# Optimization experiments

Measured on AMD Instinct MI355X. Metric: run time of the kernel, lower is better.

Reference implementation:

```python
import jax, jax.numpy as jnp
import numpy as np

B, T, D, H = 4, 4096, 4096, 128  # head_size = embedding_size // num_heads = 4096 // 32

def setup_inputs() -> dict:
    key = jax.random.key(0)
    kx, kq, kk, kv = jax.random.split(key, 4)
    x = jax.random.normal(kx, (B, T, D), dtype=jnp.float32)
    # Dense kernels (no bias), init scale 0.01 as in the module
    Wq = jax.random.normal(kq, (D, H), dtype=jnp.float32) * 0.01
    Wk = jax.random.normal(kk, (D, H), dtype=jnp.float32) * 0.01
    Wv = jax.random.normal(kv, (D, H), dtype=jnp.float32) * 0.01
    return {"x": x, "Wq": Wq, "Wk": Wk, "Wv": Wv}

def reference(x, Wq, Wk, Wv):
    # Single-head projections: (B,T,D) @ (D,H) -> (B,T,H)
    Q = jnp.einsum('btd,dh->bth', x, Wq)
    K = jnp.einsum('btd,dh->bth', x, Wk)
    V = jnp.einsum('btd,dh->bth', x, Wv)
    scale = 1.0 / jnp.sqrt(jnp.asarray(H, dtype=Q.dtype))
    scores = jnp.einsum('bth,bsh->bts', Q, K) * scale  # (B,T,S) full score matrix
    weights = jax.nn.softmax(scores, axis=-1)
    # dropout rate = 0.0 (deterministic/eval) -> identity
    out = jnp.einsum('bts,bsh->bth', weights, V)  # (B,T,H)
    return out
```

## Files before the change

kernel.cpp:

```cpp
#include <hip/hip_runtime.h>


typedef __bf16 bf16_t;
typedef bf16_t bf16x8 __attribute__((ext_vector_type(8)));
typedef float f32x4 __attribute__((ext_vector_type(4)));
typedef float f32x8 __attribute__((ext_vector_type(8)));

#define MFMA16(A, B, C) __builtin_amdgcn_mfma_f32_16x16x32_bf16((A), (B), (C), 0, 0, 0)

__device__ __forceinline__ void async_cp16(const bf16_t* g, bf16_t* lds) {
  __builtin_amdgcn_global_load_lds(
      (__attribute__((address_space(1))) unsigned int*)g,
      (__attribute__((address_space(3))) unsigned int*)lds, 16, 0, 0);
}

__global__ void tr_w(const float* __restrict__ w0, const float* __restrict__ w1,
                     const float* __restrict__ w2, bf16_t* __restrict__ wt) {
  __shared__ float tile[32][33];
  const int z = blockIdx.z;
  const float* src = (z == 0) ? w0 : (z == 1) ? w1 : w2;
  bf16_t* dst = wt + (size_t)z * 128 * 4096;
  const int c0 = blockIdx.x * 32;
  const int r0 = blockIdx.y * 32;
  const int tx = threadIdx.x, ty = threadIdx.y;
#pragma unroll
  for (int j = 0; j < 4; ++j)
    tile[ty + 8 * j][tx] = src[(size_t)(r0 + ty + 8 * j) * 128 + c0 + tx];
  __syncthreads();
#pragma unroll
  for (int j = 0; j < 4; ++j)
    dst[(size_t)(c0 + ty + 8 * j) * 4096 + r0 + tx] = (bf16_t)tile[tx][ty + 8 * j];
}

__global__ void tr_v(const bf16_t* __restrict__ v, bf16_t* __restrict__ vt) {
  __shared__ bf16_t tile[32][33];
  const int b = blockIdx.z;
  const bf16_t* src = v + (size_t)b * 4096 * 128;
  bf16_t* dst = vt + (size_t)b * 128 * 4096;
  const int c0 = blockIdx.x * 32;
  const int r0 = blockIdx.y * 32;
  const int tx = threadIdx.x, ty = threadIdx.y;
#pragma unroll
  for (int j = 0; j < 4; ++j)
    tile[ty + 8 * j][tx] = src[(size_t)(r0 + ty + 8 * j) * 128 + c0 + tx];
  __syncthreads();
#pragma unroll
  for (int j = 0; j < 4; ++j)
    dst[(size_t)(c0 + ty + 8 * j) * 4096 + r0 + tx] = tile[tx][ty + 8 * j];
}

__device__ __forceinline__ void stage_b(const bf16_t* __restrict__ wt_k,
                                        bf16_t* sBbuf, int tid) {
#pragma unroll
  for (int r = 0; r < 6; ++r) {
    int cid = r * 512 + tid;
    int n = cid >> 3, pc = cid & 7;
    int lc = pc ^ (n & 7);
    async_cp16(wt_k + (size_t)n * 4096 + lc * 8, sBbuf + (size_t)cid * 8);
  }
}

__launch_bounds__(512, 2)
__global__ void qkv_proj(const float* __restrict__ x, const bf16_t* __restrict__ wt,
                         bf16_t* __restrict__ q, bf16_t* __restrict__ k,
                         bf16_t* __restrict__ v) {
  __shared__ __align__(16) bf16_t sA[2][64 * 64];
  __shared__ __align__(16) bf16_t sB[2][384 * 64];
  const int tid = threadIdx.x;
  const int w = tid >> 6, lane = tid & 63, lq = lane & 15, quad = lane >> 4;
  const int wr = w >> 2, wc = w & 3;
  const int m0 = blockIdx.x * 64;
  const int arow = tid >> 3, apc = tid & 7;
  const int alc = apc ^ (arow & 7);
  const float* xrow = x + (size_t)(m0 + arow) * 4096 + alc * 8;

  f32x4 acc[2][6];
#pragma unroll
  for (int i = 0; i < 2; ++i)
#pragma unroll
    for (int j = 0; j < 6; ++j) acc[i][j] = (f32x4){0.f, 0.f, 0.f, 0.f};

  {
    float4 f0 = ((const float4*)xrow)[0];
    float4 f1 = ((const float4*)xrow)[1];
    stage_b(wt, sB[0], tid);
    f32x8 ff = {f0.x, f0.y, f0.z, f0.w, f1.x, f1.y, f1.z, f1.w};
    *(bf16x8*)(sA[0] + arow * 64 + apc * 8) = __builtin_convertvector(ff, bf16x8);
  }
  __syncthreads();

  for (int kt = 0; kt < 64; ++kt) {
    const int buf = kt & 1;
    float4 f0, f1;
    if (kt < 63) {
      const float* xp = xrow + (kt + 1) * 64;
      f0 = ((const float4*)xp)[0];
      f1 = ((const float4*)xp)[1];
      stage_b(wt + (kt + 1) * 64, sB[buf ^ 1], tid);
    }
#pragma unroll
    for (int ks = 0; ks < 2; ++ks) {
      bf16x8 af[2], bfr[6];
      const int cc = ks * 4 + quad;
#pragma unroll
      for (int mt = 0; mt < 2; ++mt) {
        int row = wr * 32 + mt * 16 + lq;
        af[mt] = *(const bf16x8*)(sA[buf] + row * 64 + ((cc ^ (row & 7)) << 3));
      }
#pragma unroll
      for (int nt = 0; nt < 6; ++nt) {
        int n = wc * 96 + nt * 16 + lq;
        bfr[nt] = *(const bf16x8*)(sB[buf] + n * 64 + ((cc ^ (n & 7)) << 3));
      }
#pragma unroll
      for (int mt = 0; mt < 2; ++mt)
#pragma unroll
        for (int nt = 0; nt < 6; ++nt) acc[mt][nt] = MFMA16(af[mt], bfr[nt], acc[mt][nt]);
    }
    if (kt < 63) {
      f32x8 ff = {f0.x, f0.y, f0.z, f0.w, f1.x, f1.y, f1.z, f1.w};
      *(bf16x8*)(sA[buf ^ 1] + arow * 64 + apc * 8) = __builtin_convertvector(ff, bf16x8);
    }
    __syncthreads();
  }
#pragma unroll
  for (int mt = 0; mt < 2; ++mt) {
#pragma unroll
    for (int nt = 0; nt < 6; ++nt) {
      int n = wc * 96 + nt * 16 + lq;
      bf16_t* dst;
      int nn;
      if (n < 128) { dst = q; nn = n; }
      else if (n < 256) { dst = k; nn = n - 128; }
      else { dst = v; nn = n - 256; }
#pragma unroll
      for (int r = 0; r < 4; ++r) {
        int m = m0 + wr * 32 + mt * 16 + quad * 4 + r;
        dst[(size_t)m * 128 + nn] = (bf16_t)acc[mt][nt][r];
      }
    }
  }
}

__device__ __forceinline__ void stage_kv(const bf16_t* __restrict__ ksrc,
                                         const bf16_t* __restrict__ vsrc,
                                         bf16_t* sKbuf, bf16_t* sVbuf, int tid) {
#pragma unroll
  for (int r = 0; r < 4; ++r) {
    int cid = r * 256 + tid;
    int row = cid >> 4, pc = cid & 15;
    int lc = pc ^ (row & 15);
    async_cp16(ksrc + row * 128 + lc * 8, sKbuf + (size_t)cid * 8);
  }
#pragma unroll
  for (int r = 0; r < 4; ++r) {
    int cid = r * 256 + tid;
    int h = cid >> 3, pc = cid & 7;
    int lc = pc ^ (h & 7);
    async_cp16(vsrc + (size_t)h * 4096 + lc * 8, sVbuf + (size_t)cid * 8);
  }
}

__launch_bounds__(256, 2)
__global__ void flash(const bf16_t* __restrict__ q, const bf16_t* __restrict__ kk,
                      const bf16_t* __restrict__ vt, float* __restrict__ opart,
                      float* __restrict__ mlm, float* __restrict__ mll) {
  __shared__ __align__(16) bf16_t sK[2][64 * 128];
  __shared__ __align__(16) bf16_t sV[2][128 * 64];
  __shared__ __align__(16) bf16_t sP[64 * 72];
  const int tid = threadIdx.x;
  const int w = tid >> 6, lane = tid & 63, lq = lane & 15, quad = lane >> 4;
  const int b = blockIdx.x & 3;
  const int qt = (blockIdx.x >> 2) & 63;
  const int sp = blockIdx.x >> 8;
  const int qrow0 = qt * 64;

  bf16x8 qf[4];
  {
    const bf16_t* qp = q + ((size_t)b * 4096 + qrow0 + w * 16 + lq) * 128 + quad * 8;
#pragma unroll
    for (int ks = 0; ks < 4; ++ks) qf[ks] = *(const bf16x8*)(qp + ks * 32);
  }

  f32x4 accO[8];
#pragma unroll
  for (int i = 0; i < 8; ++i) accO[i] = (f32x4){0.f, 0.f, 0.f, 0.f};
  float mrow[4] = {-1e30f, -1e30f, -1e30f, -1e30f};
  float lrow[4] = {0.f, 0.f, 0.f, 0.f};

  const bf16_t* kbase = kk + (size_t)b * 4096 * 128;
  const bf16_t* vbase = vt + (size_t)b * 128 * 4096;
  const float SCL = 0.08838834764831845f * 1.4426950408889634f;
  const int it0 = sp * 32;

  stage_kv(kbase + (size_t)it0 * 64 * 128, vbase + it0 * 64, sK[0], sV[0], tid);
  __syncthreads();

  for (int i = 0; i < 32; ++i) {
    const int buf = i & 1;
    if (i < 31)
      stage_kv(kbase + (size_t)(it0 + i + 1) * 64 * 128, vbase + (it0 + i + 1) * 64,
               sK[buf ^ 1], sV[buf ^ 1], tid);

    f32x4 accS[4];
#pragma unroll
    for (int nt = 0; nt < 4; ++nt) accS[nt] = (f32x4){0.f, 0.f, 0.f, 0.f};
    __builtin_amdgcn_s_setprio(1);
#pragma unroll
    for (int ks = 0; ks < 4; ++ks) {
      const int cc = ks * 4 + quad;
#pragma unroll
      for (int nt = 0; nt < 4; ++nt) {
        int row = nt * 16 + lq;
        bf16x8 kf = *(const bf16x8*)(sK[buf] + row * 128 + ((cc ^ (row & 15)) << 3));
        accS[nt] = MFMA16(qf[ks], kf, accS[nt]);
      }
    }
    __builtin_amdgcn_s_setprio(0);

    float mxs[4];
#pragma unroll
    for (int r = 0; r < 4; ++r) {
      float t0 = fmaxf(fmaxf(accS[0][r], accS[1][r]), fmaxf(accS[2][r], accS[3][r]));
#pragma unroll
      for (int msk = 1; msk < 16; msk <<= 1) t0 = fmaxf(t0, __shfl_xor(t0, msk));
      mxs[r] = t0 * SCL;
    }
    bool grow = (mxs[0] > mrow[0]) || (mxs[1] > mrow[1]) ||
                (mxs[2] > mrow[2]) || (mxs[3] > mrow[3]);
    if (__any(grow)) {
      float al[4];
#pragma unroll
      for (int r = 0; r < 4; ++r) {
        float mn = fmaxf(mrow[r], mxs[r]);
        al[r] = exp2f(mrow[r] - mn);
        mrow[r] = mn;
        lrow[r] *= al[r];
      }
#pragma unroll
      for (int ot = 0; ot < 8; ++ot) {
        accO[ot][0] *= al[0]; accO[ot][1] *= al[1];
        accO[ot][2] *= al[2]; accO[ot][3] *= al[3];
      }
    }
    float ps[4] = {0.f, 0.f, 0.f, 0.f};
#pragma unroll
    for (int nt = 0; nt < 4; ++nt)
#pragma unroll
      for (int r = 0; r < 4; ++r) {
        float p = exp2f(fmaf(accS[nt][r], SCL, -mrow[r]));
        accS[nt][r] = p;
        ps[r] += p;
      }
#pragma unroll
    for (int r = 0; r < 4; ++r) {
      float s = ps[r];
#pragma unroll
      for (int msk = 1; msk < 16; msk <<= 1) s += __shfl_xor(s, msk);
      lrow[r] += s;
    }

#pragma unroll
    for (int nt = 0; nt < 4; ++nt) {
      int key = nt * 16 + lq;
#pragma unroll
      for (int r = 0; r < 4; ++r) {
        int prow = w * 16 + quad * 4 + r;
        sP[prow * 72 + key] = (bf16_t)accS[nt][r];
      }
    }

    __builtin_amdgcn_s_setprio(1);
#pragma unroll
    for (int ks2 = 0; ks2 < 2; ++ks2) {
      const int cc = ks2 * 4 + quad;
      bf16x8 pf = *(const bf16x8*)(sP + (w * 16 + lq) * 72 + cc * 8);
#pragma unroll
      for (int ot = 0; ot < 8; ++ot) {
        int h = ot * 16 + lq;
        bf16x8 vf = *(const bf16x8*)(sV[buf] + h * 64 + ((cc ^ (h & 7)) << 3));
        accO[ot] = MFMA16(pf, vf, accO[ot]);
      }
    }
    __builtin_amdgcn_s_setprio(0);
    __syncthreads();
  }

  float* op = opart + ((size_t)(sp * 4 + b) * 4096 + qrow0 + w * 16) * 128;
#pragma unroll
  for (int ot = 0; ot < 8; ++ot)
#pragma unroll
    for (int r = 0; r < 4; ++r)
      op[(size_t)(quad * 4 + r) * 128 + ot * 16 + lq] = accO[ot][r];
  if (lq == 0) {
#pragma unroll
    for (int r = 0; r < 4; ++r) {
      size_t idx = (size_t)(sp * 4 + b) * 4096 + qrow0 + w * 16 + quad * 4 + r;
      mlm[idx] = mrow[r];
      mll[idx] = lrow[r];
    }
  }
}

__global__ void merge(const float* __restrict__ opart, const float* __restrict__ mlm,
                      const float* __restrict__ mll, float* __restrict__ out) {
  const int idx = blockIdx.x * 256 + threadIdx.x;
  const int h = idx & 127;
  const int row = idx >> 7;
  float m0 = mlm[row], m1 = mlm[16384 + row];
  float l0 = mll[row], l1 = mll[16384 + row];
  float M = fmaxf(m0, m1);
  float w0 = exp2f(m0 - M), w1 = exp2f(m1 - M);
  float L = w0 * l0 + w1 * l1;
  float acc = w0 * opart[(size_t)row * 128 + h] +
              w1 * opart[((size_t)16384 + row) * 128 + h];
  out[idx] = acc / L;
}

extern "C" void kernel_launch(void* const* d_in, const int* in_sizes, int n_in,
                              void* d_out, int out_size, void* d_ws, size_t ws_size,
                              hipStream_t stream) {
  (void)in_sizes; (void)n_in; (void)out_size; (void)ws_size;
  const float* x  = (const float*)d_in[0];
  const float* wq = (const float*)d_in[1];
  const float* wk = (const float*)d_in[2];
  const float* wv = (const float*)d_in[3];

  char* ws = (char*)d_ws;
  bf16_t* wt  = (bf16_t*)ws;                         ws += (size_t)384 * 4096 * 2;
  bf16_t* qb  = (bf16_t*)ws;                         ws += (size_t)16384 * 128 * 2;
  bf16_t* kb  = (bf16_t*)ws;                         ws += (size_t)16384 * 128 * 2;
  bf16_t* vb  = (bf16_t*)ws;                         ws += (size_t)16384 * 128 * 2;
  bf16_t* vtb = (bf16_t*)ws;                         ws += (size_t)16384 * 128 * 2;
  float*  opart = (float*)ws;                        ws += (size_t)2 * 16384 * 128 * 4;
  float*  mlm = (float*)ws;                          ws += (size_t)2 * 16384 * 4;
  float*  mll = (float*)ws;
  float*  ob  = (float*)d_out;

  dim3 tb(32, 8, 1);
  tr_w<<<dim3(4, 128, 3), tb, 0, stream>>>(wq, wk, wv, wt);
  qkv_proj<<<dim3(256), dim3(512), 0, stream>>>(x, wt, qb, kb, vb);
  tr_v<<<dim3(4, 128, 4), tb, 0, stream>>>(vb, vtb);
  flash<<<dim3(512), dim3(256), 0, stream>>>(qb, kb, vtb, opart, mlm, mll);
  merge<<<dim3(8192), dim3(256), 0, stream>>>(opart, mlm, mll, ob);
}
```

Before: 529.0 us.

## Split QKV projection across N halves and prefetch x two tiles ahead

The QKV projection kernel is relaunched as 512 blocks of 256 threads, with each block computing 192 of the 384 output columns, so twice as many blocks spread over the CUs. The fp32 x tile is now loaded two k-steps ahead in registers and converted into LDS one step ahead. The full __syncthreads is replaced by an explicit partial vmcnt wait plus s_barrier so outstanding x loads can stay in flight. In exchange, each x tile is read twice from global memory (once per N half), and correctness now rests on the hand-written waitcnt counts.

After: 513.8 us. -2.9%, faster.

```diff
diff --git a/kernel.cpp b/kernel.cpp
--- a/kernel.cpp
+++ b/kernel.cpp
@@ -53,26 +53,35 @@
                                         bf16_t* sBbuf, int tid) {
 #pragma unroll
   for (int r = 0; r < 6; ++r) {
-    int cid = r * 512 + tid;
+    int cid = r * 256 + tid;
     int n = cid >> 3, pc = cid & 7;
     int lc = pc ^ (n & 7);
     async_cp16(wt_k + (size_t)n * 4096 + lc * 8, sBbuf + (size_t)cid * 8);
   }
 }
 
-__launch_bounds__(512, 2)
+__launch_bounds__(256, 2)
 __global__ void qkv_proj(const float* __restrict__ x, const bf16_t* __restrict__ wt,
                          bf16_t* __restrict__ q, bf16_t* __restrict__ k,
                          bf16_t* __restrict__ v) {
   __shared__ __align__(16) bf16_t sA[2][64 * 64];
-  __shared__ __align__(16) bf16_t sB[2][384 * 64];
+  __shared__ __align__(16) bf16_t sB[2][192 * 64];
   const int tid = threadIdx.x;
   const int w = tid >> 6, lane = tid & 63, lq = lane & 15, quad = lane >> 4;
-  const int wr = w >> 2, wc = w & 3;
-  const int m0 = blockIdx.x * 64;
-  const int arow = tid >> 3, apc = tid & 7;
-  const int alc = apc ^ (arow & 7);
-  const float* xrow = x + (size_t)(m0 + arow) * 4096 + alc * 8;
+  const int wr = w >> 1, wc = w & 1;
+  const int m0 = (int)(blockIdx.x >> 1) * 64;
+  const int nb = (int)(blockIdx.x & 1) * 192;
+  const bf16_t* wtb = wt + (size_t)nb * 4096;
+
+  int arow[2], apc[2], alc[2];
+#pragma unroll
+  for (int r = 0; r < 2; ++r) {
+    int ca = r * 256 + tid;
+    arow[r] = ca >> 3;
+    apc[r] = ca & 7;
+    alc[r] = apc[r] ^ (arow[r] & 7);
+  }
+  const float* xb = x + (size_t)m0 * 4096;
 
   f32x4 acc[2][6];
 #pragma unroll
@@ -80,23 +89,47 @@
 #pragma unroll
     for (int j = 0; j < 6; ++j) acc[i][j] = (f32x4){0.f, 0.f, 0.f, 0.f};
 
-  {
-    float4 f0 = ((const float4*)xrow)[0];
-    float4 f1 = ((const float4*)xrow)[1];
-    stage_b(wt, sB[0], tid);
-    f32x8 ff = {f0.x, f0.y, f0.z, f0.w, f1.x, f1.y, f1.z, f1.w};
-    *(bf16x8*)(sA[0] + arow * 64 + apc * 8) = __builtin_convertvector(ff, bf16x8);
-  }
-  __syncthreads();
+  float4 fA[4];
+#pragma unroll
+  for (int r = 0; r < 2; ++r) {
+    const float4* p = (const float4*)(xb + (size_t)arow[r] * 4096 + alc[r] * 8);
+    fA[2 * r] = p[0];
+    fA[2 * r + 1] = p[1];
+  }
+  stage_b(wtb, sB[0], tid);
+#pragma unroll
+  for (int r = 0; r < 2; ++r) {
+    f32x8 ff = {fA[2 * r].x, fA[2 * r].y, fA[2 * r].z, fA[2 * r].w,
+                fA[2 * r + 1].x, fA[2 * r + 1].y, fA[2 * r + 1].z, fA[2 * r + 1].w};
+    *(bf16x8*)(sA[0] + arow[r] * 64 + apc[r] * 8) = __builtin_convertvector(ff, bf16x8);
+  }
+#pragma unroll
+  for (int r = 0; r < 2; ++r) {
+    const float4* p = (const float4*)(xb + (size_t)arow[r] * 4096 + 64 + alc[r] * 8);
+    fA[2 * r] = p[0];
+    fA[2 * r + 1] = p[1];
+  }
+  asm volatile("s_waitcnt vmcnt(4) lgkmcnt(0)" ::: "memory");
+  __builtin_amdgcn_s_barrier();
 
   for (int kt = 0; kt < 64; ++kt) {
     const int buf = kt & 1;
-    float4 f0, f1;
-    if (kt < 63) {
-      const float* xp = xrow + (kt + 1) * 64;
-      f0 = ((const float4*)xp)[0];
-      f1 = ((const float4*)xp)[1];
-      stage_b(wt + (kt + 1) * 64, sB[buf ^ 1], tid);
+    const int ktB = (kt < 63) ? kt + 1 : 63;
+    stage_b(wtb + ktB * 64, sB[buf ^ 1], tid);
+#pragma unroll
+    for (int r = 0; r < 2; ++r) {
+      f32x8 ff = {fA[2 * r].x, fA[2 * r].y, fA[2 * r].z, fA[2 * r].w,
+                  fA[2 * r + 1].x, fA[2 * r + 1].y, fA[2 * r + 1].z, fA[2 * r + 1].w};
+      *(bf16x8*)(sA[buf ^ 1] + arow[r] * 64 + apc[r] * 8) =
+          __builtin_convertvector(ff, bf16x8);
+    }
+    const int ktA = (kt < 62) ? kt + 2 : 63;
+#pragma unroll
+    for (int r = 0; r < 2; ++r) {
+      const float4* p =
+          (const float4*)(xb + (size_t)arow[r] * 4096 + ktA * 64 + alc[r] * 8);
+      fA[2 * r] = p[0];
+      fA[2 * r + 1] = p[1];
     }
 #pragma unroll
     for (int ks = 0; ks < 2; ++ks) {
@@ -117,17 +150,14 @@
 #pragma unroll
         for (int nt = 0; nt < 6; ++nt) acc[mt][nt] = MFMA16(af[mt], bfr[nt], acc[mt][nt]);
     }
-    if (kt < 63) {
-      f32x8 ff = {f0.x, f0.y, f0.z, f0.w, f1.x, f1.y, f1.z, f1.w};
-      *(bf16x8*)(sA[buf ^ 1] + arow * 64 + apc * 8) = __builtin_convertvector(ff, bf16x8);
-    }
-    __syncthreads();
+    asm volatile("s_waitcnt vmcnt(4) lgkmcnt(0)" ::: "memory");
+    __builtin_amdgcn_s_barrier();
   }
 #pragma unroll
   for (int mt = 0; mt < 2; ++mt) {
 #pragma unroll
     for (int nt = 0; nt < 6; ++nt) {
-      int n = wc * 96 + nt * 16 + lq;
+      int n = nb + wc * 96 + nt * 16 + lq;
       bf16_t* dst;
       int nn;
       if (n < 128) { dst = q; nn = n; }
@@ -339,7 +369,7 @@
 
   dim3 tb(32, 8, 1);
   tr_w<<<dim3(4, 128, 3), tb, 0, stream>>>(wq, wk, wv, wt);
-  qkv_proj<<<dim3(256), dim3(512), 0, stream>>>(x, wt, qb, kb, vb);
+  qkv_proj<<<dim3(512), dim3(256), 0, stream>>>(x, wt, qb, kb, vb);
   tr_v<<<dim3(4, 128, 4), tb, 0, stream>>>(vb, vtb);
   flash<<<dim3(512), dim3(256), 0, stream>>>(qb, kb, vtb, opart, mlm, mll);
   merge<<<dim3(8192), dim3(256), 0, stream>>>(opart, mlm, mll, ob);
```

## Load A fragments directly to registers and triple-buffer B with explicit waitcnts

Applied to the files above, without the earlier changes.

The QKV projection kernel stops staging x through LDS. Each lane now loads its own MFMA A-fragment fp32 values straight from global memory into registers one k-step ahead and converts them to bf16 there. The weight tiles move to a three-stage LDS ring prefetched two k-steps ahead, synchronised with hand-placed s_waitcnt vmcnt counters and raw s_barrier instead of __syncthreads. This removes the A-tile LDS round trip and is meant to deepen load/compute overlap. The cost is higher LDS use (3x48KB, which may limit occupancy to one block per CU), more registers, and fragile manual vmcnt accounting.

Result: slower. 555.3 us (+5.0%).

```diff
diff --git a/kernel.cpp b/kernel.cpp
--- a/kernel.cpp
+++ b/kernel.cpp
@@ -64,15 +64,16 @@
 __global__ void qkv_proj(const float* __restrict__ x, const bf16_t* __restrict__ wt,
                          bf16_t* __restrict__ q, bf16_t* __restrict__ k,
                          bf16_t* __restrict__ v) {
-  __shared__ __align__(16) bf16_t sA[2][64 * 64];
-  __shared__ __align__(16) bf16_t sB[2][384 * 64];
+  __shared__ __align__(16) bf16_t sB[3][384 * 64];
   const int tid = threadIdx.x;
   const int w = tid >> 6, lane = tid & 63, lq = lane & 15, quad = lane >> 4;
   const int wr = w >> 2, wc = w & 3;
   const int m0 = blockIdx.x * 64;
-  const int arow = tid >> 3, apc = tid & 7;
-  const int alc = apc ^ (arow & 7);
-  const float* xrow = x + (size_t)(m0 + arow) * 4096 + alc * 8;
+
+  const float* abase[2];
+#pragma unroll
+  for (int mt = 0; mt < 2; ++mt)
+    abase[mt] = x + (size_t)(m0 + wr * 32 + mt * 16 + lq) * 4096 + quad * 8;
 
   f32x4 acc[2][6];
 #pragma unroll
@@ -80,49 +81,69 @@
 #pragma unroll
     for (int j = 0; j < 6; ++j) acc[i][j] = (f32x4){0.f, 0.f, 0.f, 0.f};
 
-  {
-    float4 f0 = ((const float4*)xrow)[0];
-    float4 f1 = ((const float4*)xrow)[1];
-    stage_b(wt, sB[0], tid);
-    f32x8 ff = {f0.x, f0.y, f0.z, f0.w, f1.x, f1.y, f1.z, f1.w};
-    *(bf16x8*)(sA[0] + arow * 64 + apc * 8) = __builtin_convertvector(ff, bf16x8);
-  }
-  __syncthreads();
-
+  float4 fAr[8];
+#define LOADA(KT)                                                         \
+  {                                                                       \
+    _Pragma("unroll") for (int mt = 0; mt < 2; ++mt) {                    \
+      _Pragma("unroll") for (int ks = 0; ks < 2; ++ks) {                  \
+        const float4* p = (const float4*)(abase[mt] + (KT)*64 + ks * 32); \
+        fAr[(mt * 2 + ks) * 2 + 0] = p[0];                                \
+        fAr[(mt * 2 + ks) * 2 + 1] = p[1];                                \
+      }                                                                   \
+    }                                                                     \
+  }
+
+  stage_b(wt, sB[0], tid);
+  __builtin_amdgcn_sched_barrier(0);
+  LOADA(0);
+  __builtin_amdgcn_sched_barrier(0);
+  stage_b(wt + 64, sB[1], tid);
+  __builtin_amdgcn_sched_barrier(0);
+  asm volatile("s_waitcnt vmcnt(14)" ::: "memory");
+  __builtin_amdgcn_s_barrier();
+
+  int cur = 0;
   for (int kt = 0; kt < 64; ++kt) {
-    const int buf = kt & 1;
-    float4 f0, f1;
-    if (kt < 63) {
-      const float* xp = xrow + (kt + 1) * 64;
-      f0 = ((const float4*)xp)[0];
-      f1 = ((const float4*)xp)[1];
-      stage_b(wt + (kt + 1) * 64, sB[buf ^ 1], tid);
-    }
+    asm volatile("s_waitcnt vmcnt(6)" ::: "memory");
+    __builtin_amdgcn_sched_barrier(0);
+    bf16x8 af[2][2];
+#pragma unroll
+    for (int mt = 0; mt < 2; ++mt)
+#pragma unroll
+      for (int ks = 0; ks < 2; ++ks) {
+        float4 a = fAr[(mt * 2 + ks) * 2 + 0], b = fAr[(mt * 2 + ks) * 2 + 1];
+        f32x8 ff = {a.x, a.y, a.z, a.w, b.x, b.y, b.z, b.w};
+        af[mt][ks] = __builtin_convertvector(ff, bf16x8);
+      }
+    const int ktA = (kt < 63) ? kt + 1 : 63;
+    LOADA(ktA);
+    __builtin_amdgcn_sched_barrier(0);
+    const int ktB = (kt < 62) ? kt + 2 : 63;
+    const int stg = (cur < 1) ? cur + 2 : cur - 1;
+    stage_b(wt + ktB * 64, sB[stg], tid);
+    __builtin_amdgcn_sched_barrier(0);
+    const bf16_t* sBc = sB[cur];
 #pragma unroll
     for (int ks = 0; ks < 2; ++ks) {
-      bf16x8 af[2], bfr[6];
+      bf16x8 bfr[6];
       const int cc = ks * 4 + quad;
-#pragma unroll
-      for (int mt = 0; mt < 2; ++mt) {
-        int row = wr * 32 + mt * 16 + lq;
-        af[mt] = *(const bf16x8*)(sA[buf] + row * 64 + ((cc ^ (row & 7)) << 3));
-      }
 #pragma unroll
       for (int nt = 0; nt < 6; ++nt) {
         int n = wc * 96 + nt * 16 + lq;
-        bfr[nt] = *(const bf16x8*)(sB[buf] + n * 64 + ((cc ^ (n & 7)) << 3));
+        bfr[nt] = *(const bf16x8*)(sBc + n * 64 + ((cc ^ (n & 7)) << 3));
       }
 #pragma unroll
       for (int mt = 0; mt < 2; ++mt)
 #pragma unroll
-        for (int nt = 0; nt < 6; ++nt) acc[mt][nt] = MFMA16(af[mt], bfr[nt], acc[mt][nt]);
-    }
-    if (kt < 63) {
-      f32x8 ff = {f0.x, f0.y, f0.z, f0.w, f1.x, f1.y, f1.z, f1.w};
-      *(bf16x8*)(sA[buf ^ 1] + arow * 64 + apc * 8) = __builtin_convertvector(ff, bf16x8);
-    }
-    __syncthreads();
-  }
+        for (int nt = 0; nt < 6; ++nt)
+          acc[mt][nt] = MFMA16(af[mt][ks], bfr[nt], acc[mt][nt]);
+    }
+    asm volatile("s_waitcnt vmcnt(14) lgkmcnt(0)" ::: "memory");
+    __builtin_amdgcn_s_barrier();
+    cur = (cur < 2) ? cur + 1 : 0;
+  }
+#undef LOADA
+
 #pragma unroll
   for (int mt = 0; mt < 2; ++mt) {
 #pragma unroll
```

## Compute transposed QKV projection to write V^T directly and drop tr_v kernel

Applied to the files above, without the earlier changes.

The projection kernel is rewritten so that weights act as the A operand and x as the B operand, producing W^T x^T tiles. x is loaded straight from global memory into registers, converted to bf16 and fed to MFMA with no LDS staging. This lets V be written already transposed (global layout [128][16384]), which removes the separate tr_v kernel and its intermediate buffer. Q and K are written with packed bf16x4 stores. The flash kernel's V addressing is updated to the new stride. The trade-offs are occupancy reduced to one 512-thread block per CU, custom waitcnt/barrier handling, and scattered 2-byte stores for V^T.

Result: no change. 539.3 us (+2.0%).

```diff
diff --git a/kernel.cpp b/kernel.cpp
--- a/kernel.cpp
+++ b/kernel.cpp
@@ -2,6 +2,7 @@
 
 
 typedef __bf16 bf16_t;
+typedef bf16_t bf16x4 __attribute__((ext_vector_type(4)));
 typedef bf16_t bf16x8 __attribute__((ext_vector_type(8)));
 typedef float f32x4 __attribute__((ext_vector_type(4)));
 typedef float f32x8 __attribute__((ext_vector_type(8)));
@@ -32,111 +33,107 @@
     dst[(size_t)(c0 + ty + 8 * j) * 4096 + r0 + tx] = (bf16_t)tile[tx][ty + 8 * j];
 }
 
-__global__ void tr_v(const bf16_t* __restrict__ v, bf16_t* __restrict__ vt) {
-  __shared__ bf16_t tile[32][33];
-  const int b = blockIdx.z;
-  const bf16_t* src = v + (size_t)b * 4096 * 128;
-  bf16_t* dst = vt + (size_t)b * 128 * 4096;
-  const int c0 = blockIdx.x * 32;
-  const int r0 = blockIdx.y * 32;
-  const int tx = threadIdx.x, ty = threadIdx.y;
-#pragma unroll
-  for (int j = 0; j < 4; ++j)
-    tile[ty + 8 * j][tx] = src[(size_t)(r0 + ty + 8 * j) * 128 + c0 + tx];
-  __syncthreads();
-#pragma unroll
-  for (int j = 0; j < 4; ++j)
-    dst[(size_t)(c0 + ty + 8 * j) * 4096 + r0 + tx] = tile[tx][ty + 8 * j];
-}
-
-__device__ __forceinline__ void stage_b(const bf16_t* __restrict__ wt_k,
-                                        bf16_t* sBbuf, int tid) {
+__device__ __forceinline__ void stage_w(const bf16_t* __restrict__ wt_k,
+                                        bf16_t* sWbuf, int tid) {
 #pragma unroll
   for (int r = 0; r < 6; ++r) {
     int cid = r * 512 + tid;
     int n = cid >> 3, pc = cid & 7;
     int lc = pc ^ (n & 7);
-    async_cp16(wt_k + (size_t)n * 4096 + lc * 8, sBbuf + (size_t)cid * 8);
-  }
-}
-
-__launch_bounds__(512, 2)
-__global__ void qkv_proj(const float* __restrict__ x, const bf16_t* __restrict__ wt,
-                         bf16_t* __restrict__ q, bf16_t* __restrict__ k,
-                         bf16_t* __restrict__ v) {
-  __shared__ __align__(16) bf16_t sA[2][64 * 64];
-  __shared__ __align__(16) bf16_t sB[2][384 * 64];
+    async_cp16(wt_k + (size_t)n * 4096 + lc * 8, sWbuf + (size_t)cid * 8);
+  }
+}
+
+__launch_bounds__(512, 1)
+__global__ void qkv_t(const float* __restrict__ x, const bf16_t* __restrict__ wt,
+                      bf16_t* __restrict__ q, bf16_t* __restrict__ k,
+                      bf16_t* __restrict__ vt) {
+  __shared__ __align__(16) bf16_t sW[2][384 * 64];
   const int tid = threadIdx.x;
   const int w = tid >> 6, lane = tid & 63, lq = lane & 15, quad = lane >> 4;
-  const int wr = w >> 2, wc = w & 3;
-  const int m0 = blockIdx.x * 64;
-  const int arow = tid >> 3, apc = tid & 7;
-  const int alc = apc ^ (arow & 7);
-  const float* xrow = x + (size_t)(m0 + arow) * 4096 + alc * 8;
-
-  f32x4 acc[2][6];
-#pragma unroll
-  for (int i = 0; i < 2; ++i)
-#pragma unroll
-    for (int j = 0; j < 6; ++j) acc[i][j] = (f32x4){0.f, 0.f, 0.f, 0.f};
-
-  {
-    float4 f0 = ((const float4*)xrow)[0];
-    float4 f1 = ((const float4*)xrow)[1];
-    stage_b(wt, sB[0], tid);
-    f32x8 ff = {f0.x, f0.y, f0.z, f0.w, f1.x, f1.y, f1.z, f1.w};
-    *(bf16x8*)(sA[0] + arow * 64 + apc * 8) = __builtin_convertvector(ff, bf16x8);
-  }
-  __syncthreads();
+  const int wr = w >> 1, wc = w & 1;
+  const int t0 = blockIdx.x * 64;
+
+  const float* xb[2];
+#pragma unroll
+  for (int nt = 0; nt < 2; ++nt)
+    xb[nt] = x + (size_t)(t0 + wc * 32 + nt * 16 + lq) * 4096 + quad * 8;
+
+  f32x4 acc[6][2];
+#pragma unroll
+  for (int i = 0; i < 6; ++i)
+#pragma unroll
+    for (int j = 0; j < 2; ++j) acc[i][j] = (f32x4){0.f, 0.f, 0.f, 0.f};
+
+  float4 fX[8];
+#define LOADX(KT)                                                    \
+  {                                                                  \
+    _Pragma("unroll") for (int nt = 0; nt < 2; ++nt) {               \
+      _Pragma("unroll") for (int ks = 0; ks < 2; ++ks) {             \
+        const float4* p = (const float4*)(xb[nt] + (KT)*64 + ks*32); \
+        fX[(nt * 2 + ks) * 2 + 0] = p[0];                            \
+        fX[(nt * 2 + ks) * 2 + 1] = p[1];                            \
+      }                                                              \
+    }                                                                \
+  }
+
+  stage_w(wt, sW[0], tid);
+  LOADX(0);
+  asm volatile("s_waitcnt vmcnt(8)" ::: "memory");
+  __builtin_amdgcn_s_barrier();
 
   for (int kt = 0; kt < 64; ++kt) {
     const int buf = kt & 1;
-    float4 f0, f1;
-    if (kt < 63) {
-      const float* xp = xrow + (kt + 1) * 64;
-      f0 = ((const float4*)xp)[0];
-      f1 = ((const float4*)xp)[1];
-      stage_b(wt + (kt + 1) * 64, sB[buf ^ 1], tid);
-    }
+    const int ktW = (kt < 63) ? kt + 1 : 63;
+    stage_w(wt + ktW * 64, sW[buf ^ 1], tid);
+    bf16x8 bfr[4];
+#pragma unroll
+    for (int nt = 0; nt < 2; ++nt)
+#pragma unroll
+      for (int ks = 0; ks < 2; ++ks) {
+        float4 a = fX[(nt * 2 + ks) * 2 + 0], b = fX[(nt * 2 + ks) * 2 + 1];
+        f32x8 ff = {a.x, a.y, a.z, a.w, b.x, b.y, b.z, b.w};
+        bfr[nt * 2 + ks] = __builtin_convertvector(ff, bf16x8);
+      }
+    const int ktX = (kt < 63) ? kt + 1 : 63;
+    LOADX(ktX);
 #pragma unroll
     for (int ks = 0; ks < 2; ++ks) {
-      bf16x8 af[2], bfr[6];
       const int cc = ks * 4 + quad;
-#pragma unroll
-      for (int mt = 0; mt < 2; ++mt) {
-        int row = wr * 32 + mt * 16 + lq;
-        af[mt] = *(const bf16x8*)(sA[buf] + row * 64 + ((cc ^ (row & 7)) << 3));
-      }
-#pragma unroll
-      for (int nt = 0; nt < 6; ++nt) {
-        int n = wc * 96 + nt * 16 + lq;
-        bfr[nt] = *(const bf16x8*)(sB[buf] + n * 64 + ((cc ^ (n & 7)) << 3));
-      }
-#pragma unroll
-      for (int mt = 0; mt < 2; ++mt)
-#pragma unroll
-        for (int nt = 0; nt < 6; ++nt) acc[mt][nt] = MFMA16(af[mt], bfr[nt], acc[mt][nt]);
-    }
-    if (kt < 63) {
-      f32x8 ff = {f0.x, f0.y, f0.z, f0.w, f1.x, f1.y, f1.z, f1.w};
-      *(bf16x8*)(sA[buf ^ 1] + arow * 64 + apc * 8) = __builtin_convertvector(ff, bf16x8);
-    }
-    __syncthreads();
-  }
-#pragma unroll
-  for (int mt = 0; mt < 2; ++mt) {
-#pragma unroll
-    for (int nt = 0; nt < 6; ++nt) {
-      int n = wc * 96 + nt * 16 + lq;
-      bf16_t* dst;
-      int nn;
-      if (n < 128) { dst = q; nn = n; }
-      else if (n < 256) { dst = k; nn = n - 128; }
-      else { dst = v; nn = n - 256; }
-#pragma unroll
-      for (int r = 0; r < 4; ++r) {
-        int m = m0 + wr * 32 + mt * 16 + quad * 4 + r;
-        dst[(size_t)m * 128 + nn] = (bf16_t)acc[mt][nt][r];
+      bf16x8 af[6];
+#pragma unroll
+      for (int mt = 0; mt < 6; ++mt) {
+        int n = wr * 96 + mt * 16 + lq;
+        af[mt] = *(const bf16x8*)(sW[buf] + n * 64 + ((cc ^ (n & 7)) << 3));
+      }
+#pragma unroll
+      for (int mt = 0; mt < 6; ++mt)
+#pragma unroll
+        for (int nt = 0; nt < 2; ++nt)
+          acc[mt][nt] = MFMA16(af[mt], bfr[nt * 2 + ks], acc[mt][nt]);
+    }
+    asm volatile("s_waitcnt vmcnt(8) lgkmcnt(0)" ::: "memory");
+    __builtin_amdgcn_s_barrier();
+  }
+#undef LOADX
+
+#pragma unroll
+  for (int mt = 0; mt < 6; ++mt) {
+    const int hg0 = wr * 96 + mt * 16 + quad * 4;
+#pragma unroll
+    for (int nt = 0; nt < 2; ++nt) {
+      const int t = t0 + wc * 32 + nt * 16 + lq;
+      if (hg0 < 256) {
+        bf16_t* dst = (hg0 < 128) ? (q + (size_t)t * 128 + hg0)
+                                  : (k + (size_t)t * 128 + (hg0 - 128));
+        bf16x4 pk;
+#pragma unroll
+        for (int r = 0; r < 4; ++r) pk[r] = (bf16_t)acc[mt][nt][r];
+        *(bf16x4*)dst = pk;
+      } else {
+#pragma unroll
+        for (int r = 0; r < 4; ++r)
+          vt[(size_t)(hg0 - 256 + r) * 16384 + t] = (bf16_t)acc[mt][nt][r];
       }
     }
   }
@@ -157,7 +154,7 @@
     int cid = r * 256 + tid;
     int h = cid >> 3, pc = cid & 7;
     int lc = pc ^ (h & 7);
-    async_cp16(vsrc + (size_t)h * 4096 + lc * 8, sVbuf + (size_t)cid * 8);
+    async_cp16(vsrc + (size_t)h * 16384 + lc * 8, sVbuf + (size_t)cid * 8);
   }
 }
 
@@ -189,7 +186,7 @@
   float lrow[4] = {0.f, 0.f, 0.f, 0.f};
 
   const bf16_t* kbase = kk + (size_t)b * 4096 * 128;
-  const bf16_t* vbase = vt + (size_t)b * 128 * 4096;
+  const bf16_t* vbase = vt + (size_t)b * 4096;
   const float SCL = 0.08838834764831845f * 1.4426950408889634f;
   const int it0 = sp * 32;
 
@@ -330,7 +327,6 @@
   bf16_t* wt  = (bf16_t*)ws;                         ws += (size_t)384 * 4096 * 2;
   bf16_t* qb  = (bf16_t*)ws;                         ws += (size_t)16384 * 128 * 2;
   bf16_t* kb  = (bf16_t*)ws;                         ws += (size_t)16384 * 128 * 2;
-  bf16_t* vb  = (bf16_t*)ws;                         ws += (size_t)16384 * 128 * 2;
   bf16_t* vtb = (bf16_t*)ws;                         ws += (size_t)16384 * 128 * 2;
   float*  opart = (float*)ws;                        ws += (size_t)2 * 16384 * 128 * 4;
   float*  mlm = (float*)ws;                          ws += (size_t)2 * 16384 * 4;
@@ -339,8 +335,7 @@
 
   dim3 tb(32, 8, 1);
   tr_w<<<dim3(4, 128, 3), tb, 0, stream>>>(wq, wk, wv, wt);
-  qkv_proj<<<dim3(256), dim3(512), 0, stream>>>(x, wt, qb, kb, vb);
-  tr_v<<<dim3(4, 128, 4), tb, 0, stream>>>(vb, vtb);
+  qkv_t<<<dim3(256), dim3(512), 0, stream>>>(x, wt, qb, kb, vtb);
   flash<<<dim3(512), dim3(256), 0, stream>>>(qb, kb, vtb, opart, mlm, mll);
   merge<<<dim3(8192), dim3(256), 0, stream>>>(opart, mlm, mll, ob);
 }
```
